# Kernel tuning notes

Hardware: AMD Instinct MI355X
Metric: run time of the kernel (lower is better)

The kernel has to match this reference:

```python
import jax, jax.numpy as jnp
import numpy as np

N_USER = 100000
N_ITEM = 200000
N_NODES = N_USER + N_ITEM
NNZ = 4000000
EMB = 64
N_LAYERS = 3
BATCH = 4096


def setup_inputs() -> dict:
    key = jax.random.key(0)
    ks = jax.random.split(key, 12)
    inp = {
        'users': jax.random.randint(ks[0], (BATCH,), 0, N_USER, dtype=jnp.int32),
        'pos_items': jax.random.randint(ks[1], (BATCH,), 0, N_ITEM, dtype=jnp.int32),
        'neg_items': jax.random.randint(ks[2], (BATCH,), 0, N_ITEM, dtype=jnp.int32),
        'row': jax.random.randint(ks[3], (NNZ,), 0, N_NODES, dtype=jnp.int32),
        'col': jax.random.randint(ks[4], (NNZ,), 0, N_NODES, dtype=jnp.int32),
        'vals': jax.random.uniform(ks[5], (NNZ,), dtype=jnp.float32),
        'user_emb': 0.1 * jax.random.normal(ks[6], (N_USER, EMB), dtype=jnp.float32),
        'item_emb': 0.1 * jax.random.normal(ks[7], (N_ITEM, EMB), dtype=jnp.float32),
        'W_gc': 0.1 * jax.random.normal(ks[8], (N_LAYERS, EMB, EMB), dtype=jnp.float32),
        'b_gc': 0.1 * jax.random.normal(ks[9], (N_LAYERS, EMB), dtype=jnp.float32),
        'W_bi': 0.1 * jax.random.normal(ks[10], (N_LAYERS, EMB, EMB), dtype=jnp.float32),
        'b_bi': 0.1 * jax.random.normal(ks[11], (N_LAYERS, EMB), dtype=jnp.float32),
    }
    return inp


def _l2_normalize(x, eps=1e-12):
    # matches torch F.normalize(p=2, dim=1): x / max(||x||, eps)
    n = jnp.sqrt(jnp.sum(x * x, axis=1, keepdims=True))
    return x / jnp.maximum(n, eps)


def reference(users, pos_items, neg_items, row, col, vals, user_emb, item_emb, W_gc, b_gc, W_bi, b_bi):
    B = users.shape[0]
    # sparse adjacency propagation: side = A_hat @ [user_emb; item_emb]
    emb = jnp.concatenate([user_emb, item_emb], axis=0)          # [N, d]
    msgs = vals[:, None] * emb[col]                               # [nnz, d]
    side = jax.ops.segment_sum(msgs, row, num_segments=N_NODES)  # [N, d]

    u_side = side[users]                                          # [B, d]
    i_side = jnp.concatenate([side[N_USER + pos_items], side[N_USER + neg_items]], axis=0)
    small_side = jnp.concatenate([u_side, i_side], axis=0)        # [3B, d]
    ego = jnp.concatenate([user_emb[users], item_emb[pos_items], item_emb[neg_items]], axis=0)

    all_embeddings = [ego]
    for k in range(N_LAYERS):
        sum_e = small_side @ W_gc[k] + b_gc[k]
        bi = (ego * small_side) @ W_bi[k] + b_bi[k]
        ego = jax.nn.leaky_relu(sum_e + bi, negative_slope=0.2)
        all_embeddings.append(_l2_normalize(ego))

    all_e = jnp.concatenate(all_embeddings, axis=1)               # [3B, d*(L+1)]
    u_g = all_e[:B]
    i_g = all_e[B:]
    pos_g = i_g[:B]
    neg_g = i_g[B:]
    return (u_g, pos_g, neg_g)
```

## Files before the change

### kernel.cpp

```cpp
#include <hip/hip_runtime.h>

#define N_USER   100000
#define N_ITEM   200000
#define N_NODES  300000
#define NNZ      4000000
#define EMB      64
#define N_LAYERS 3
#define BATCH    4096
#define NSLOT    (3*BATCH)
#define MAXE     96
#define HCAP     768


#define TBL4   37500
#define CNT4   3072

__global__ void __launch_bounds__(256) k_clear(int4* __restrict__ table4,
                                               int4* __restrict__ count4) {
    int i = blockIdx.x * blockDim.x + threadIdx.x;
    if (i < TBL4)              table4[i] = make_int4(-1, -1, -1, -1);
    else if (i < TBL4 + CNT4)  count4[i - TBL4] = make_int4(0, 0, 0, 0);
}

__global__ void k_setup(const int* __restrict__ users,
                        const int* __restrict__ pos,
                        const int* __restrict__ neg,
                        unsigned short* __restrict__ table16) {
    int i = blockIdx.x * blockDim.x + threadIdx.x;
    if (i >= NSLOT) return;
    int node;
    if (i < BATCH)            node = users[i];
    else if (i < 2 * BATCH)   node = N_USER + pos[i - BATCH];
    else                      node = N_USER + neg[i - 2 * BATCH];
    table16[node] = (unsigned short)i;
}

__global__ void __launch_bounds__(256) k_build(
        const int* __restrict__ row,
        const int* __restrict__ col,
        const float* __restrict__ vals,
        const unsigned short* __restrict__ table16,
        int* __restrict__ count,
        int2* __restrict__ csr2) {
    __shared__ int   ls_s[HCAP];
    __shared__ int   ls_c[HCAP];
    __shared__ float ls_v[HCAP];
    __shared__ int   cnt;
    int tid = threadIdx.x;
    if (tid == 0) cnt = 0;
    __syncthreads();

    const int4*   rows4 = (const int4*)row;
    const int4*   cols4 = (const int4*)col;
    const float4* vals4 = (const float4*)vals;
    const int nt4 = NNZ / 4;
    int base4 = blockIdx.x * 512;

    int4 r[2], c[2]; float4 v[2]; bool ok[2];
    #pragma unroll
    for (int q = 0; q < 2; ++q) {
        int t = base4 + q * 256 + tid;
        ok[q] = t < nt4;
        int tt = ok[q] ? t : 0;
        r[q] = rows4[tt];
        c[q] = cols4[tt];
        v[q] = vals4[tt];
    }
    int s[8];
    #pragma unroll
    for (int q = 0; q < 2; ++q) {
        s[q * 4 + 0] = (int)(short)table16[r[q].x];
        s[q * 4 + 1] = (int)(short)table16[r[q].y];
        s[q * 4 + 2] = (int)(short)table16[r[q].z];
        s[q * 4 + 3] = (int)(short)table16[r[q].w];
    }
    #pragma unroll
    for (int q = 0; q < 2; ++q) {
        if (!ok[q]) continue;
        int cc[4] = { c[q].x, c[q].y, c[q].z, c[q].w };
        float vv[4] = { v[q].x, v[q].y, v[q].z, v[q].w };
        #pragma unroll
        for (int i = 0; i < 4; ++i) {
            int si = s[q * 4 + i];
            if (si >= 0) {
                int p = atomicAdd(&cnt, 1);
                if (p < HCAP) { ls_s[p] = si; ls_c[p] = cc[i]; ls_v[p] = vv[i]; }
                else {
                    int pp = atomicAdd(&count[si], 1);
                    if (pp < MAXE)
                        csr2[(size_t)si * MAXE + pp] = make_int2(cc[i], __float_as_int(vv[i]));
                }
            }
        }
    }
    __syncthreads();

    int n = cnt; n = (n < HCAP) ? n : HCAP;
    for (int t = tid; t < n; t += 256) {
        int si = ls_s[t];
        int p = atomicAdd(&count[si], 1);
        if (p < MAXE)
            csr2[(size_t)si * MAXE + p] = make_int2(ls_c[t], __float_as_int(ls_v[t]));
    }
}

__global__ void __launch_bounds__(256) k_gather(
        const int* __restrict__ users,
        const int* __restrict__ pos,
        const int* __restrict__ neg,
        const float* __restrict__ user_emb,
        const float* __restrict__ item_emb,
        const unsigned short* __restrict__ table16,
        const int* __restrict__ count,
        const int2* __restrict__ csr2,
        float* __restrict__ side) {
    int tid = threadIdx.x;
    int w = tid >> 6;
    int j = tid & 63;
    int slot = blockIdx.x * 4 + w;

    int node;
    if (slot < BATCH)          node = users[slot];
    else if (slot < 2 * BATCH) node = N_USER + pos[slot - BATCH];
    else                       node = N_USER + neg[slot - 2 * BATCH];

    int wslot = (int)(short)table16[node];
    wslot = __builtin_amdgcn_readfirstlane(wslot);
    int n = count[wslot];
    n = (n < MAXE) ? n : MAXE;
    n = __builtin_amdgcn_readfirstlane(n);
    const int2* base = csr2 + (size_t)wslot * MAXE;

    float acc = 0.f;
    for (int t0 = 0; t0 < n; t0 += 64) {
        int idx = t0 + j;
        int2 ev = make_int2(0, 0);
        if (idx < n) ev = base[idx];
        int m = n - t0; m = (m < 64) ? m : 64;
        for (int tt = 0; tt < m; tt += 16) {
            float vv[16], gg[16];
            #pragma unroll
            for (int k = 0; k < 16; ++k) {
                int  t  = tt + k;
                bool okk = t < m;
                int   cc = __shfl(ev.x, t, 64);
                float vb = __uint_as_float((unsigned)__shfl(ev.y, t, 64));
                vv[k] = okk ? vb : 0.f;
                int ci = okk ? cc : 0;
                const float* sp = (ci < N_USER) ? (user_emb + (size_t)ci * EMB)
                                                : (item_emb + (size_t)(ci - N_USER) * EMB);
                gg[k] = sp[j];
            }
            #pragma unroll
            for (int k = 0; k < 16; ++k) acc = fmaf(vv[k], gg[k], acc);
        }
    }
    side[(size_t)slot * EMB + j] = acc;
}

__global__ void __launch_bounds__(256) k_mlp(
        const int* __restrict__ users,
        const int* __restrict__ pos,
        const int* __restrict__ neg,
        const float* __restrict__ user_emb,
        const float* __restrict__ item_emb,
        const float* __restrict__ W_gc,
        const float* __restrict__ b_gc,
        const float* __restrict__ W_bi,
        const float* __restrict__ b_bi,
        const float* __restrict__ side,
        float* __restrict__ out) {
    __shared__ float wg[EMB * EMB];
    __shared__ float wb[EMB * EMB];
    int tid = threadIdx.x;
    int w = tid >> 6;
    int j = tid & 63;
    int sbase = blockIdx.x * 16 + w * 4;

    float sval[4], e[4];
    #pragma unroll
    for (int s = 0; s < 4; ++s) {
        int slot = sbase + s;
        int node;
        if (slot < BATCH)          node = users[slot];
        else if (slot < 2 * BATCH) node = N_USER + pos[slot - BATCH];
        else                       node = N_USER + neg[slot - 2 * BATCH];
        const float* erow = (node < N_USER) ? (user_emb + (size_t)node * EMB)
                                            : (item_emb + (size_t)(node - N_USER) * EMB);
        e[s]    = erow[j];
        sval[s] = side[(size_t)slot * EMB + j];
        out[(size_t)slot * 256 + j] = e[s];
    }

    for (int k = 0; k < N_LAYERS; ++k) {
        __syncthreads();
        {
            const float4* g4 = (const float4*)(W_gc + (size_t)k * EMB * EMB);
            const float4* b4 = (const float4*)(W_bi + (size_t)k * EMB * EMB);
            float4* lg = (float4*)wg;
            float4* lb = (float4*)wb;
            #pragma unroll
            for (int i2 = tid; i2 < EMB * EMB / 4; i2 += 256) { lg[i2] = g4[i2]; lb[i2] = b4[i2]; }
        }
        __syncthreads();

        float b1 = b_gc[k * EMB + j];
        float b2 = b_bi[k * EMB + j];
        float sum1[4], sum2[4], pv[4];
        #pragma unroll
        for (int s = 0; s < 4; ++s) { sum1[s] = b1; sum2[s] = b2; pv[s] = sval[s] * e[s]; }

        #pragma unroll 8
        for (int i = 0; i < EMB; ++i) {
            float wgi = wg[i * EMB + j];
            float wbi = wb[i * EMB + j];
            #pragma unroll
            for (int s = 0; s < 4; ++s) {
                float si = __uint_as_float(__builtin_amdgcn_readlane(__float_as_uint(sval[s]), i));
                float pi = __uint_as_float(__builtin_amdgcn_readlane(__float_as_uint(pv[s]),   i));
                sum1[s] = fmaf(si, wgi, sum1[s]);
                sum2[s] = fmaf(pi, wbi, sum2[s]);
            }
        }

        #pragma unroll
        for (int s = 0; s < 4; ++s) {
            float x = sum1[s] + sum2[s];
            x = (x >= 0.f) ? x : 0.2f * x;
            float sq = x * x;
            #pragma unroll
            for (int o = 32; o; o >>= 1) sq += __shfl_xor(sq, o, 64);
            float nn = fmaxf(sqrtf(sq), 1e-12f);
            out[(size_t)(sbase + s) * 256 + (k + 1) * 64 + j] = x / nn;
            e[s] = x;
        }
    }
}

extern "C" void kernel_launch(void* const* d_in, const int* in_sizes, int n_in,
                              void* d_out, int out_size, void* d_ws, size_t ws_size,
                              hipStream_t stream) {
    const int*   users    = (const int*)  d_in[0];
    const int*   pos      = (const int*)  d_in[1];
    const int*   neg      = (const int*)  d_in[2];
    const int*   row      = (const int*)  d_in[3];
    const int*   col      = (const int*)  d_in[4];
    const float* vals     = (const float*)d_in[5];
    const float* user_emb = (const float*)d_in[6];
    const float* item_emb = (const float*)d_in[7];
    const float* W_gc     = (const float*)d_in[8];
    const float* b_gc     = (const float*)d_in[9];
    const float* W_bi     = (const float*)d_in[10];
    const float* b_bi     = (const float*)d_in[11];
    float* out = (float*)d_out;

    char* ws = (char*)d_ws;
    unsigned short* table16 = (unsigned short*)ws;
    int*            count   = (int*)(ws + 600064);
    int2*           csr2    = (int2*)(ws + 649216);
    float*          side    = (float*)(ws + 10086400);

    k_clear<<<(TBL4 + CNT4 + 255) / 256, 256, 0, stream>>>((int4*)table16, (int4*)count);
    k_setup<<<(NSLOT + 255) / 256, 256, 0, stream>>>(users, pos, neg, table16);
    k_build<<<(NNZ / 4 + 511) / 512, 256, 0, stream>>>(row, col, vals, table16,
                                                       count, csr2);
    k_gather<<<NSLOT / 4, 256, 0, stream>>>(users, pos, neg, user_emb, item_emb,
                                            table16, count, csr2, side);
    k_mlp<<<NSLOT / 16, 256, 0, stream>>>(users, pos, neg, user_emb, item_emb,
                                          W_gc, b_gc, W_bi, b_bi, side, out);
}
```

Measured before the change: 81.87 us.

## Split CSR build into row-only scan and sparse col/val fill pass

The single build kernel streamed row, col and vals for every nonzero. It is replaced by a scan kernel that reads only row indices plus the slot table and writes per-block hit lists of (edge index, slot). A second fill kernel then fetches col and vals only for the hits and appends them to the CSR with atomics. Because only a small fraction of edges hit the batch nodes, this avoids reading most of the col and vals arrays. The cost is an extra launch, a hit-list round trip, and scattered reads of col and vals.

```diff
diff --git a/kernel.cpp b/kernel.cpp
--- a/kernel.cpp
+++ b/kernel.cpp
@@ -9,17 +9,21 @@
 #define BATCH    4096
 #define NSLOT    (3*BATCH)
 #define MAXE     96
-#define HCAP     768
+#define SLABS    3907
+#define SLABCAP  128
 
 
 #define TBL4   37500
 #define CNT4   3072
-
-__global__ void __launch_bounds__(256) k_clear(int4* __restrict__ table4,
-                                               int4* __restrict__ count4) {
+#define SCNT4  1024
+
+__global__ void __launch_bounds__(256) k_clear(int4* __restrict__ t4,
+                                               int4* __restrict__ c4,
+                                               int4* __restrict__ s4) {
     int i = blockIdx.x * blockDim.x + threadIdx.x;
-    if (i < TBL4)              table4[i] = make_int4(-1, -1, -1, -1);
-    else if (i < TBL4 + CNT4)  count4[i - TBL4] = make_int4(0, 0, 0, 0);
+    if (i < TBL4)                     t4[i] = make_int4(-1, -1, -1, -1);
+    else if (i < TBL4 + CNT4)         c4[i - TBL4] = make_int4(0, 0, 0, 0);
+    else if (i < TBL4 + CNT4 + SCNT4) s4[i - TBL4 - CNT4] = make_int4(0, 0, 0, 0);
 }
 
 __global__ void k_setup(const int* __restrict__ users,
@@ -35,73 +39,68 @@
     table16[node] = (unsigned short)i;
 }
 
-__global__ void __launch_bounds__(256) k_build(
+__global__ void __launch_bounds__(256) k_scan(
         const int* __restrict__ row,
+        const unsigned short* __restrict__ table16,
         const int* __restrict__ col,
         const float* __restrict__ vals,
-        const unsigned short* __restrict__ table16,
         int* __restrict__ count,
-        int2* __restrict__ csr2) {
-    __shared__ int   ls_s[HCAP];
-    __shared__ int   ls_c[HCAP];
-    __shared__ float ls_v[HCAP];
-    __shared__ int   cnt;
+        int2* __restrict__ csr2,
+        int* __restrict__ slabcnt,
+        int2* __restrict__ hitlist) {
+    __shared__ int2 lh[SLABCAP];
+    __shared__ int cnt;
     int tid = threadIdx.x;
     if (tid == 0) cnt = 0;
     __syncthreads();
 
-    const int4*   rows4 = (const int4*)row;
-    const int4*   cols4 = (const int4*)col;
-    const float4* vals4 = (const float4*)vals;
-    const int nt4 = NNZ / 4;
-    int base4 = blockIdx.x * 512;
-
-    int4 r[2], c[2]; float4 v[2]; bool ok[2];
-    #pragma unroll
-    for (int q = 0; q < 2; ++q) {
-        int t = base4 + q * 256 + tid;
-        ok[q] = t < nt4;
-        int tt = ok[q] ? t : 0;
-        r[q] = rows4[tt];
-        c[q] = cols4[tt];
-        v[q] = vals4[tt];
-    }
-    int s[8];
-    #pragma unroll
-    for (int q = 0; q < 2; ++q) {
-        s[q * 4 + 0] = (int)(short)table16[r[q].x];
-        s[q * 4 + 1] = (int)(short)table16[r[q].y];
-        s[q * 4 + 2] = (int)(short)table16[r[q].z];
-        s[q * 4 + 3] = (int)(short)table16[r[q].w];
-    }
-    #pragma unroll
-    for (int q = 0; q < 2; ++q) {
-        if (!ok[q]) continue;
-        int cc[4] = { c[q].x, c[q].y, c[q].z, c[q].w };
-        float vv[4] = { v[q].x, v[q].y, v[q].z, v[q].w };
+    int t = blockIdx.x * 256 + tid;
+    if (t < NNZ / 4) {
+        int4 r = ((const int4*)row)[t];
+        int ss[4];
+        ss[0] = (int)(short)table16[r.x];
+        ss[1] = (int)(short)table16[r.y];
+        ss[2] = (int)(short)table16[r.z];
+        ss[3] = (int)(short)table16[r.w];
+        int e = t * 4;
         #pragma unroll
         for (int i = 0; i < 4; ++i) {
-            int si = s[q * 4 + i];
-            if (si >= 0) {
+            if (ss[i] >= 0) {
                 int p = atomicAdd(&cnt, 1);
-                if (p < HCAP) { ls_s[p] = si; ls_c[p] = cc[i]; ls_v[p] = vv[i]; }
+                if (p < SLABCAP) lh[p] = make_int2(e + i, ss[i]);
                 else {
-                    int pp = atomicAdd(&count[si], 1);
+                    int pp = atomicAdd(&count[ss[i]], 1);
                     if (pp < MAXE)
-                        csr2[(size_t)si * MAXE + pp] = make_int2(cc[i], __float_as_int(vv[i]));
+                        csr2[(size_t)ss[i] * MAXE + pp] =
+                            make_int2(col[e + i], __float_as_int(vals[e + i]));
                 }
             }
         }
     }
     __syncthreads();
-
-    int n = cnt; n = (n < HCAP) ? n : HCAP;
-    for (int t = tid; t < n; t += 256) {
-        int si = ls_s[t];
-        int p = atomicAdd(&count[si], 1);
-        if (p < MAXE)
-            csr2[(size_t)si * MAXE + p] = make_int2(ls_c[t], __float_as_int(ls_v[t]));
-    }
+    int n = cnt; n = (n < SLABCAP) ? n : SLABCAP;
+    if (tid < n) hitlist[(size_t)blockIdx.x * SLABCAP + tid] = lh[tid];
+    if (tid == 0) slabcnt[blockIdx.x] = n;
+}
+
+__global__ void __launch_bounds__(256) k_fill(
+        const int* __restrict__ col,
+        const float* __restrict__ vals,
+        const int* __restrict__ slabcnt,
+        const int2* __restrict__ hitlist,
+        int* __restrict__ count,
+        int2* __restrict__ csr2) {
+    int idx = blockIdx.x * 256 + threadIdx.x;
+    if (idx >= SLABS * SLABCAP) return;
+    int s = idx >> 7;
+    int i = idx & (SLABCAP - 1);
+    if (i >= slabcnt[s]) return;
+    int2 h = hitlist[idx];
+    int   c = col[h.x];
+    float v = vals[h.x];
+    int p = atomicAdd(&count[h.y], 1);
+    if (p < MAXE)
+        csr2[(size_t)h.y * MAXE + p] = make_int2(c, __float_as_int(v));
 }
 
 __global__ void __launch_bounds__(256) k_gather(
@@ -259,11 +258,16 @@
     int*            count   = (int*)(ws + 600064);
     int2*           csr2    = (int2*)(ws + 649216);
     float*          side    = (float*)(ws + 10086400);
-
-    k_clear<<<(TBL4 + CNT4 + 255) / 256, 256, 0, stream>>>((int4*)table16, (int4*)count);
+    int*            slabcnt = (int*)(ws + 13232128);
+    int2*           hitlist = (int2*)(ws + 13248512);
+
+    k_clear<<<(TBL4 + CNT4 + SCNT4 + 255) / 256, 256, 0, stream>>>(
+        (int4*)table16, (int4*)count, (int4*)slabcnt);
     k_setup<<<(NSLOT + 255) / 256, 256, 0, stream>>>(users, pos, neg, table16);
-    k_build<<<(NNZ / 4 + 511) / 512, 256, 0, stream>>>(row, col, vals, table16,
-                                                       count, csr2);
+    k_scan<<<SLABS, 256, 0, stream>>>(row, table16, col, vals, count, csr2,
+                                      slabcnt, hitlist);
+    k_fill<<<(SLABS * SLABCAP + 255) / 256, 256, 0, stream>>>(
+        col, vals, slabcnt, hitlist, count, csr2);
     k_gather<<<NSLOT / 4, 256, 0, stream>>>(users, pos, neg, user_emb, item_emb,
                                             table16, count, csr2, side);
     k_mlp<<<NSLOT / 16, 256, 0, stream>>>(users, pos, neg, user_emb, item_emb,
```

Measured after the change: 89.32 us. 9.1% more time.

## Replace dense slot table clear with membership bitmap for edge filtering

Applied to the files above, without the earlier changes.

A 37.5KB bitmap marks which nodes are in the batch, so the 600KB 16-bit slot table no longer has to be cleared to -1 each call. The edge-scan kernel tests the bitmap first and reads table16 only for hits. It also processes one int4 per thread with smaller blocks and a smaller shared staging buffer. The aim is to cut the clear traffic and the scattered table lookups. In exchange, setup now does atomicOr writes and table16 keeps stale entries, which are safe only because they are read solely for nodes flagged in the bitmap.

```diff
diff --git a/kernel.cpp b/kernel.cpp
--- a/kernel.cpp
+++ b/kernel.cpp
@@ -9,23 +9,25 @@
 #define BATCH    4096
 #define NSLOT    (3*BATCH)
 #define MAXE     96
-#define HCAP     768
-
-
-#define TBL4   37500
+#define HCAP     256
+#define BMWORDS  9376
+
+
 #define CNT4   3072
-
-__global__ void __launch_bounds__(256) k_clear(int4* __restrict__ table4,
-                                               int4* __restrict__ count4) {
+#define BM4    2344
+
+__global__ void __launch_bounds__(256) k_clear(int4* __restrict__ c4,
+                                               int4* __restrict__ b4) {
     int i = blockIdx.x * blockDim.x + threadIdx.x;
-    if (i < TBL4)              table4[i] = make_int4(-1, -1, -1, -1);
-    else if (i < TBL4 + CNT4)  count4[i - TBL4] = make_int4(0, 0, 0, 0);
+    if (i < CNT4)            c4[i] = make_int4(0, 0, 0, 0);
+    else if (i < CNT4 + BM4) b4[i - CNT4] = make_int4(0, 0, 0, 0);
 }
 
 __global__ void k_setup(const int* __restrict__ users,
                         const int* __restrict__ pos,
                         const int* __restrict__ neg,
-                        unsigned short* __restrict__ table16) {
+                        unsigned short* __restrict__ table16,
+                        unsigned int* __restrict__ bitmap) {
     int i = blockIdx.x * blockDim.x + threadIdx.x;
     if (i >= NSLOT) return;
     int node;
@@ -33,12 +35,14 @@
     else if (i < 2 * BATCH)   node = N_USER + pos[i - BATCH];
     else                      node = N_USER + neg[i - 2 * BATCH];
     table16[node] = (unsigned short)i;
+    atomicOr(&bitmap[((unsigned)node) >> 5], 1u << (node & 31));
 }
 
 __global__ void __launch_bounds__(256) k_build(
         const int* __restrict__ row,
         const int* __restrict__ col,
         const float* __restrict__ vals,
+        const unsigned int* __restrict__ bitmap,
         const unsigned short* __restrict__ table16,
         int* __restrict__ count,
         int2* __restrict__ csr2) {
@@ -50,39 +54,23 @@
     if (tid == 0) cnt = 0;
     __syncthreads();
 
-    const int4*   rows4 = (const int4*)row;
-    const int4*   cols4 = (const int4*)col;
-    const float4* vals4 = (const float4*)vals;
-    const int nt4 = NNZ / 4;
-    int base4 = blockIdx.x * 512;
-
-    int4 r[2], c[2]; float4 v[2]; bool ok[2];
-    #pragma unroll
-    for (int q = 0; q < 2; ++q) {
-        int t = base4 + q * 256 + tid;
-        ok[q] = t < nt4;
-        int tt = ok[q] ? t : 0;
-        r[q] = rows4[tt];
-        c[q] = cols4[tt];
-        v[q] = vals4[tt];
-    }
-    int s[8];
-    #pragma unroll
-    for (int q = 0; q < 2; ++q) {
-        s[q * 4 + 0] = (int)(short)table16[r[q].x];
-        s[q * 4 + 1] = (int)(short)table16[r[q].y];
-        s[q * 4 + 2] = (int)(short)table16[r[q].z];
-        s[q * 4 + 3] = (int)(short)table16[r[q].w];
-    }
-    #pragma unroll
-    for (int q = 0; q < 2; ++q) {
-        if (!ok[q]) continue;
-        int cc[4] = { c[q].x, c[q].y, c[q].z, c[q].w };
-        float vv[4] = { v[q].x, v[q].y, v[q].z, v[q].w };
+    int t = blockIdx.x * 256 + tid;
+    if (t < NNZ / 4) {
+        int4   r = ((const int4*)row)[t];
+        int4   c = ((const int4*)col)[t];
+        float4 v = ((const float4*)vals)[t];
+        bool h0 = (bitmap[((unsigned)r.x) >> 5] >> (r.x & 31)) & 1;
+        bool h1 = (bitmap[((unsigned)r.y) >> 5] >> (r.y & 31)) & 1;
+        bool h2 = (bitmap[((unsigned)r.z) >> 5] >> (r.z & 31)) & 1;
+        bool h3 = (bitmap[((unsigned)r.w) >> 5] >> (r.w & 31)) & 1;
+        int rr[4] = { r.x, r.y, r.z, r.w };
+        int cc[4] = { c.x, c.y, c.z, c.w };
+        float vv[4] = { v.x, v.y, v.z, v.w };
+        bool hh[4] = { h0, h1, h2, h3 };
         #pragma unroll
         for (int i = 0; i < 4; ++i) {
-            int si = s[q * 4 + i];
-            if (si >= 0) {
+            if (hh[i]) {
+                int si = (int)table16[rr[i]];
                 int p = atomicAdd(&cnt, 1);
                 if (p < HCAP) { ls_s[p] = si; ls_c[p] = cc[i]; ls_v[p] = vv[i]; }
                 else {
@@ -96,11 +84,11 @@
     __syncthreads();
 
     int n = cnt; n = (n < HCAP) ? n : HCAP;
-    for (int t = tid; t < n; t += 256) {
-        int si = ls_s[t];
+    for (int t2 = tid; t2 < n; t2 += 256) {
+        int si = ls_s[t2];
         int p = atomicAdd(&count[si], 1);
         if (p < MAXE)
-            csr2[(size_t)si * MAXE + p] = make_int2(ls_c[t], __float_as_int(ls_v[t]));
+            csr2[(size_t)si * MAXE + p] = make_int2(ls_c[t2], __float_as_int(ls_v[t2]));
     }
 }
 
@@ -124,7 +112,7 @@
     else if (slot < 2 * BATCH) node = N_USER + pos[slot - BATCH];
     else                       node = N_USER + neg[slot - 2 * BATCH];
 
-    int wslot = (int)(short)table16[node];
+    int wslot = (int)table16[node];
     wslot = __builtin_amdgcn_readfirstlane(wslot);
     int n = count[wslot];
     n = (n < MAXE) ? n : MAXE;
@@ -259,11 +247,12 @@
     int*            count   = (int*)(ws + 600064);
     int2*           csr2    = (int2*)(ws + 649216);
     float*          side    = (float*)(ws + 10086400);
-
-    k_clear<<<(TBL4 + CNT4 + 255) / 256, 256, 0, stream>>>((int4*)table16, (int4*)count);
-    k_setup<<<(NSLOT + 255) / 256, 256, 0, stream>>>(users, pos, neg, table16);
-    k_build<<<(NNZ / 4 + 511) / 512, 256, 0, stream>>>(row, col, vals, table16,
-                                                       count, csr2);
+    unsigned int*   bitmap  = (unsigned int*)(ws + 13232128);
+
+    k_clear<<<(CNT4 + BM4 + 255) / 256, 256, 0, stream>>>((int4*)count, (int4*)bitmap);
+    k_setup<<<(NSLOT + 255) / 256, 256, 0, stream>>>(users, pos, neg, table16, bitmap);
+    k_build<<<(NNZ / 4 + 255) / 256, 256, 0, stream>>>(row, col, vals, bitmap,
+                                                       table16, count, csr2);
     k_gather<<<NSLOT / 4, 256, 0, stream>>>(users, pos, neg, user_emb, item_emb,
                                             table16, count, csr2, side);
     k_mlp<<<NSLOT / 16, 256, 0, stream>>>(users, pos, neg, user_emb, item_emb,
```

Measured after the change: 76.79 us. -6.2%, faster.
